# Kernel tuning notes

Measured on AMD Instinct MI355X. Metric: run time of the kernel, lower is better.

The kernel has to match this reference:

```python
import jax, jax.numpy as jnp
import numpy as np

N = 8192      # total nodes = B * NPG
D = 512       # in_dim = hidden_dim = out_dim
E = 131072    # edges
B = 16        # graphs (selected_idx batch)
NPG = 512     # nodes per graph
S = 128       # selected nodes per graph
L = 3         # conv layers
EPS = 1e-5


def setup_inputs() -> dict:
    key = jax.random.key(0)
    ks = jax.random.split(key, 16)
    scale = 0.02
    return {
        "x": jax.random.normal(ks[0], (N, D), dtype=jnp.float32),
        "edge_index": jax.random.randint(ks[1], (2, E), 0, N),
        "selected_idx": jax.random.randint(ks[2], (B, S), 0, NPG),
        "edge_label": jax.random.randint(ks[3], (E,), 0, 4),
        # per-layer EdgeConv MLP params (stacked over L layers)
        "conv_W1": jax.random.normal(ks[4], (L, 2 * D, D), dtype=jnp.float32) * scale,
        "conv_b1": jnp.full((L, D), 0.01, dtype=jnp.float32),
        "conv_W2": jax.random.normal(ks[5], (L, D, D), dtype=jnp.float32) * scale,
        "conv_b2": jnp.full((L, D), 0.01, dtype=jnp.float32),
        # shared layer norms
        "ln1_g": jnp.ones((D,), dtype=jnp.float32),
        "ln1_b": jnp.zeros((D,), dtype=jnp.float32),
        "ln2_g": jnp.ones((D,), dtype=jnp.float32),
        "ln2_b": jnp.zeros((D,), dtype=jnp.float32),
        # final FFN
        "ffn_W1": jax.random.normal(ks[6], (D, D), dtype=jnp.float32) * scale,
        "ffn_b1": jnp.full((D,), 0.01, dtype=jnp.float32),
        "ffn_W2": jax.random.normal(ks[7], (D, D), dtype=jnp.float32) * scale,
        "ffn_b2": jnp.full((D,), 0.01, dtype=jnp.float32),
    }


def _layer_norm(x, g, b):
    mu = jnp.mean(x, axis=-1, keepdims=True)
    var = jnp.mean(jnp.square(x - mu), axis=-1, keepdims=True)
    return (x - mu) * jax.lax.rsqrt(var + EPS) * g + b


def reference(x, edge_index, selected_idx, edge_label,
              conv_W1, conv_b1, conv_W2, conv_b2,
              ln1_g, ln1_b, ln2_g, ln2_b,
              ffn_W1, ffn_b1, ffn_W2, ffn_b2):
    src = edge_index[0]  # x_j source nodes
    dst = edge_index[1]  # x_i target nodes (aggregation index)
    for l in range(L):
        residual = x
        h = _layer_norm(x, ln1_g, ln1_b)
        hi = h[dst]                                   # [E, D]
        hj = h[src]                                   # [E, D]
        ef = jnp.concatenate([hi, hj - hi], axis=1)   # [E, 2D]
        m = jnp.maximum(ef @ conv_W1[l] + conv_b1[l], 0.0) @ conv_W2[l] + conv_b2[l]
        agg = jax.ops.segment_max(m, dst, num_segments=N)  # max-aggregate [N, D]
        agg = jnp.where(jnp.isfinite(agg), agg, 0.0)       # nodes w/o in-edges -> 0
        x = jnp.maximum(agg, 0.0) + residual
    residual = x
    h = _layer_norm(x, ln2_g, ln2_b)
    y = jnp.maximum(h @ ffn_W1 + ffn_b1, 0.0) @ ffn_W2 + ffn_b2
    x = y + residual
    x = x.reshape(B, NPG, D)
    idx = jnp.broadcast_to(selected_idx[:, :, None], (B, S, D))
    return jnp.take_along_axis(x, idx, axis=1)  # [B, S, D]
```

## Files before the change

### kernel.cpp

```cpp
#include <hip/hip_runtime.h>
#include <stdint.h>

#define NN 8192
#define DD 512
#define EE 131072
#define BBATCH 16
#define NPG 512
#define SSEL 128
#define LL 3

typedef unsigned short u16;
typedef __bf16 bf16x8 __attribute__((ext_vector_type(8)));
typedef float f32x4 __attribute__((ext_vector_type(4)));
typedef float f32x2 __attribute__((ext_vector_type(2)));
typedef u16 u16x8 __attribute__((ext_vector_type(8)));

__device__ __forceinline__ float bf2f(u16 u) {
    union { unsigned i; float f; } v; v.i = ((unsigned)u) << 16; return v.f;
}
__device__ __forceinline__ u16 f2bf(float f) {
    union { unsigned i; float f; } v; v.f = f;
    unsigned i = v.i;
    return (u16)((i + 0x7FFFu + ((i >> 16) & 1u)) >> 16);
}

__device__ __forceinline__ unsigned pk_bf16(float s0, float s1) {
#if __has_builtin(__builtin_amdgcn_cvt_pk_bf16_f32)
    typedef __bf16 bf16x2 __attribute__((ext_vector_type(2)));
    union { bf16x2 v; unsigned u; } r;
    r.v = __builtin_amdgcn_cvt_pk_bf16_f32(s0, s1);
    return r.u;
#else
    unsigned r0 = __float_as_uint(s0);
    r0 = (r0 + 0x7FFFu + ((r0 >> 16) & 1u)) >> 16;
    unsigned r1 = __float_as_uint(s1);
    r1 = (r1 + 0x7FFFu + ((r1 >> 16) & 1u)) & 0xffff0000u;
    return r0 | r1;
#endif
}

__device__ __forceinline__ void async_cp16(const u16* g, u16* l) {
    __builtin_amdgcn_global_load_lds(
        (const __attribute__((address_space(1))) unsigned int*)g,
        (__attribute__((address_space(3))) unsigned int*)l, 16, 0, 0);
}

__global__ __launch_bounds__(256) void ln_fused(const float* __restrict__ xin,
                                                float* __restrict__ agg_io,
                                                float* __restrict__ xout,
                                                const float* __restrict__ g,
                                                const float* __restrict__ b,
                                                u16* __restrict__ h, int doAdd) {
    int row = blockIdx.x * 4 + (threadIdx.x >> 6);
    int lane = threadIdx.x & 63;
    const f32x4* x4 = (const f32x4*)(xin + (size_t)row * DD);
    f32x4 p = x4[lane * 2], q = x4[lane * 2 + 1];
    if (doAdd) {
        const f32x4* a4 = (const f32x4*)(agg_io + (size_t)row * DD);
        f32x4 pa = a4[lane * 2], qa = a4[lane * 2 + 1];
        #pragma unroll
        for (int i = 0; i < 4; ++i) { p[i] += pa[i]; q[i] += qa[i]; }
    }
    if (agg_io) {
        f32x4 z;
        #pragma unroll
        for (int i = 0; i < 4; ++i) z[i] = 0.f;
        f32x4* a4 = (f32x4*)(agg_io + (size_t)row * DD);
        a4[lane * 2] = z;
        a4[lane * 2 + 1] = z;
    }
    f32x4* xo = (f32x4*)(xout + (size_t)row * DD);
    xo[lane * 2] = p;
    xo[lane * 2 + 1] = q;
    float v[8];
    v[0] = p[0]; v[1] = p[1]; v[2] = p[2]; v[3] = p[3];
    v[4] = q[0]; v[5] = q[1]; v[6] = q[2]; v[7] = q[3];
    float s = 0.f, sq = 0.f;
    #pragma unroll
    for (int i = 0; i < 8; ++i) { s += v[i]; sq += v[i] * v[i]; }
    #pragma unroll
    for (int o = 32; o >= 1; o >>= 1) { s += __shfl_xor(s, o); sq += __shfl_xor(sq, o); }
    float mu = s * (1.f / DD);
    float var = sq * (1.f / DD) - mu * mu;
    float rs = rsqrtf(var + 1e-5f);
    int kb = lane * 8;
    u16x8 o8;
    #pragma unroll
    for (int i = 0; i < 8; ++i) o8[i] = f2bf((v[i] - mu) * rs * g[kb + i] + b[kb + i]);
    *(u16x8*)(h + (size_t)row * DD + kb) = o8;
}

__global__ __launch_bounds__(256) void ln_sel(const float* __restrict__ x,
                                              const float* __restrict__ agg,
                                              const int* __restrict__ sel,
                                              const float* __restrict__ g,
                                              const float* __restrict__ b,
                                              float* __restrict__ xs,
                                              u16* __restrict__ hs) {
    int i = blockIdx.x * 4 + (threadIdx.x >> 6);
    int lane = threadIdx.x & 63;
    int r = (i >> 7) * NPG + sel[i];
    const f32x4* x4 = (const f32x4*)(x + (size_t)r * DD);
    const f32x4* a4 = (const f32x4*)(agg + (size_t)r * DD);
    f32x4 p = x4[lane * 2], q = x4[lane * 2 + 1];
    f32x4 pa = a4[lane * 2], qa = a4[lane * 2 + 1];
    #pragma unroll
    for (int j = 0; j < 4; ++j) { p[j] += pa[j]; q[j] += qa[j]; }
    f32x4* xo = (f32x4*)(xs + (size_t)i * DD);
    xo[lane * 2] = p;
    xo[lane * 2 + 1] = q;
    float v[8];
    v[0] = p[0]; v[1] = p[1]; v[2] = p[2]; v[3] = p[3];
    v[4] = q[0]; v[5] = q[1]; v[6] = q[2]; v[7] = q[3];
    float s = 0.f, sq = 0.f;
    #pragma unroll
    for (int j = 0; j < 8; ++j) { s += v[j]; sq += v[j] * v[j]; }
    #pragma unroll
    for (int o = 32; o >= 1; o >>= 1) { s += __shfl_xor(s, o); sq += __shfl_xor(sq, o); }
    float mu = s * (1.f / DD);
    float var = sq * (1.f / DD) - mu * mu;
    float rs = rsqrtf(var + 1e-5f);
    int kb = lane * 8;
    u16x8 o8;
    #pragma unroll
    for (int j = 0; j < 8; ++j) o8[j] = f2bf((v[j] - mu) * rs * g[kb + j] + b[kb + j]);
    *(u16x8*)(hs + (size_t)i * DD + kb) = o8;
}

__global__ void hist_kernel(const int* __restrict__ dst, int* __restrict__ cnt) {
    int e = blockIdx.x * 256 + threadIdx.x;
    if (e < EE) atomicAdd(&cnt[dst[e]], 1);
}

__global__ __launch_bounds__(1024) void scan_kernel(const int* __restrict__ cnt,
                                                    int* __restrict__ off,
                                                    int* __restrict__ cur) {
    __shared__ int part[1024];
    int t = threadIdx.x;
    int base = t * 8;
    int loc[8]; int s = 0;
    #pragma unroll
    for (int i = 0; i < 8; ++i) { loc[i] = s; s += cnt[base + i]; }
    part[t] = s;
    __syncthreads();
    for (int o = 1; o < 1024; o <<= 1) {
        int v = part[t];
        int u = (t >= o) ? part[t - o] : 0;
        __syncthreads();
        part[t] = v + u;
        __syncthreads();
    }
    int bx = (t > 0) ? part[t - 1] : 0;
    #pragma unroll
    for (int i = 0; i < 8; ++i) { off[base + i] = bx + loc[i]; cur[base + i] = bx + loc[i]; }
    if (t == 0) off[NN] = part[1023];
}

__global__ void scatter_kernel(const int* __restrict__ src, const int* __restrict__ dst,
                               int* __restrict__ cur, int* __restrict__ ssrc,
                               int* __restrict__ sdst) {
    int e = blockIdx.x * 256 + threadIdx.x;
    if (e < EE) {
        int d = dst[e];
        int p = atomicAdd(&cur[d], 1);
        ssrc[p] = src[e];
        sdst[p] = d;
    }
}

struct CvtJobs {
    const float* s[5];
    u16* d[5];
};
__global__ __launch_bounds__(256) void cvt_t5_kernel(CvtJobs jobs) {
    __shared__ u16 tile[32][33];
    const float* src = jobs.s[blockIdx.z];
    u16* dstp = jobs.d[blockIdx.z];
    int bk = blockIdx.x * 32, bn = blockIdx.y * 32;
    int tx = threadIdx.x & 31, ty = threadIdx.x >> 5;
    #pragma unroll
    for (int r = 0; r < 32; r += 8)
        tile[ty + r][tx] = f2bf(src[(size_t)(bk + ty + r) * 512 + bn + tx]);
    __syncthreads();
    #pragma unroll
    for (int r = 0; r < 32; r += 8)
        dstp[(size_t)(bn + ty + r) * 512 + bk + tx] = tile[tx][ty + r];
}

__global__ __launch_bounds__(256) void cvt_w1_kernel(const float* __restrict__ W1g,
                                                     u16* __restrict__ dstg) {
    __shared__ u16 tile[32][33];
    const float* W1 = W1g + (size_t)blockIdx.z * 1024 * 512;
    u16* dstp = dstg + (size_t)blockIdx.z * 1024 * 512;
    int bk = blockIdx.x * 32, bn = blockIdx.y * 32;
    int tx = threadIdx.x & 31, ty = threadIdx.x >> 5;
    #pragma unroll
    for (int r = 0; r < 32; r += 8) {
        int k = bk + ty + r, n = bn + tx;
        float v = (n < 512) ? (W1[(size_t)k * 512 + n] - W1[(size_t)(k + 512) * 512 + n])
                            : W1[(size_t)(k + 512) * 512 + (n - 512)];
        tile[ty + r][tx] = f2bf(v);
    }
    __syncthreads();
    #pragma unroll
    for (int r = 0; r < 32; r += 8)
        dstp[(size_t)(bn + ty + r) * 512 + bk + tx] = tile[tx][ty + r];
}

template <int EMODE>
__global__ __launch_bounds__(256) void gemm_async(
    const u16* __restrict__ A, const u16* __restrict__ BT,
    const float* __restrict__ bias, const float* __restrict__ resid,
    void* __restrict__ Cout, int K, int ldc) {
    __shared__ u16 lA[128 * 64];
    __shared__ u16 lB[128 * 64];
    const int tid = threadIdx.x;
    const int lane = tid & 63, wave = tid >> 6;
    const int wm = wave & 1, wn = wave >> 1;
    const int quad = lane >> 4, lm = lane & 15;
    const int tileM = blockIdx.x, tileN = blockIdx.y;

    const int g = (lane & 7) ^ (lane >> 3);
    const u16* ap[4];
    const u16* bp[4];
    u16* lad[4];
    u16* lbd[4];
    #pragma unroll
    for (int j = 0; j < 4; ++j) {
        int seg = wave * 4 + j;
        int rA = tileM * 128 + seg * 8 + (lane >> 3);
        int rB = tileN * 128 + seg * 8 + (lane >> 3);
        ap[j] = A + (size_t)rA * K + g * 8;
        bp[j] = BT + (size_t)rB * K + g * 8;
        lad[j] = lA + seg * 512;
        lbd[j] = lB + seg * 512;
    }

    f32x4 acc[4][4];
    #pragma unroll
    for (int mt = 0; mt < 4; ++mt)
        #pragma unroll
        for (int nt = 0; nt < 4; ++nt)
            #pragma unroll
            for (int j = 0; j < 4; ++j) acc[mt][nt][j] = 0.f;

    for (int kb = 0; kb < K; kb += 64) {
        #pragma unroll
        for (int j = 0; j < 4; ++j) {
            async_cp16(ap[j], lad[j]);
            async_cp16(bp[j], lbd[j]);
            ap[j] += 64;
            bp[j] += 64;
        }
        __syncthreads();
        #pragma unroll
        for (int kk = 0; kk < 64; kk += 32) {
            bf16x8 af[4], bfr[4];
            int gbase = (kk >> 3) + quad;
            #pragma unroll
            for (int mt = 0; mt < 4; ++mt) {
                int row = wm * 64 + mt * 16 + lm;
                af[mt] = *(const bf16x8*)(lA + row * 64 + ((gbase ^ (row & 7)) << 3));
            }
            #pragma unroll
            for (int nt = 0; nt < 4; ++nt) {
                int row = wn * 64 + nt * 16 + lm;
                bfr[nt] = *(const bf16x8*)(lB + row * 64 + ((gbase ^ (row & 7)) << 3));
            }
            #pragma unroll
            for (int mt = 0; mt < 4; ++mt)
                #pragma unroll
                for (int nt = 0; nt < 4; ++nt)
                    acc[mt][nt] = __builtin_amdgcn_mfma_f32_16x16x32_bf16(
                        af[mt], bfr[nt], acc[mt][nt], 0, 0, 0);
        }
        __syncthreads();
    }
    #pragma unroll
    for (int mt = 0; mt < 4; ++mt) {
        #pragma unroll
        for (int nt = 0; nt < 4; ++nt) {
            int col = tileN * 128 + wn * 64 + nt * 16 + lm;
            float bv;
            if (EMODE == 2) bv = 0.f;
            else if (EMODE == 3) bv = (col < 512) ? bias[col] : 0.f;
            else bv = bias[col];
            #pragma unroll
            for (int j = 0; j < 4; ++j) {
                int grow = tileM * 128 + wm * 64 + mt * 16 + quad * 4 + j;
                float v = acc[mt][nt][j] + bv;
                if (EMODE == 0) {
                    ((u16*)Cout)[(size_t)grow * ldc + col] = f2bf(fmaxf(v, 0.f));
                } else if (EMODE == 1) {
                    ((float*)Cout)[(size_t)grow * ldc + col] =
                        v + resid[(size_t)grow * ldc + col];
                } else {
                    ((u16*)Cout)[(size_t)grow * ldc + col] = f2bf(v);
                }
            }
        }
    }
}

__global__ __launch_bounds__(1024, 4) void gemm_edge(
    const u16* __restrict__ P, const int* __restrict__ ssrc,
    const int* __restrict__ sdst, const u16* __restrict__ W2T,
    const float* __restrict__ b2, float* __restrict__ agg) {
    __shared__ u16 smem[128 * 64 + 512 * 64];
    __shared__ int nid_l[128];
    u16* lA = smem;
    u16* lB = smem + 128 * 64;
    const int tid = threadIdx.x;
    const int lane = tid & 63, wave = tid >> 6;
    const int wm = wave >> 3, wn = wave & 7;
    const int quad = lane >> 4, lm = lane & 15;
    const int ebase = blockIdx.x * 128;

    if (tid < 128) nid_l[tid] = sdst[ebase + tid];

    const int g = (lane & 7) ^ (lane >> 3);
    int aoff, boff, lout;
    {
        int row = wave * 8 + (lane >> 3);
        int dn = sdst[ebase + row];
        int sn = ssrc[ebase + row];
        aoff = dn * 1024 + g * 8;
        boff = sn * 1024 + 512 + g * 8;
        lout = wave * 512 + lane * 8;
    }
    int wbase, lbbase;
    {
        int row0 = wave * 32 + (lane >> 3);
        wbase = row0 * 512 + g * 8;
        lbbase = wave * 2048;
    }

    f32x4 acc[4][4];
    #pragma unroll
    for (int mt = 0; mt < 4; ++mt)
        #pragma unroll
        for (int nt = 0; nt < 4; ++nt)
            #pragma unroll
            for (int j = 0; j < 4; ++j) acc[mt][nt][j] = 0.f;

    for (int kb = 0; kb < 512; kb += 64) {
        u16x8 ga = *(const u16x8*)(P + aoff + kb);
        u16x8 gb = *(const u16x8*)(P + boff + kb);
        #pragma unroll
        for (int j = 0; j < 4; ++j)
            async_cp16(W2T + wbase + j * 4096 + kb, lB + lbbase + j * 512);
        {
            union { u16x8 v; unsigned w[4]; } ua, ub;
            ua.v = ga;
            ub.v = gb;
            unsigned o[4];
            #pragma unroll
            for (int q = 0; q < 4; ++q) {
                f32x2 a, c;
                a[0] = __uint_as_float(ua.w[q] << 16);
                a[1] = __uint_as_float(ua.w[q] & 0xffff0000u);
                c[0] = __uint_as_float(ub.w[q] << 16);
                c[1] = __uint_as_float(ub.w[q] & 0xffff0000u);
                f32x2 s = a + c;
#if __has_builtin(__builtin_elementwise_max)
                f32x2 z; z[0] = 0.f; z[1] = 0.f;
                s = __builtin_elementwise_max(s, z);
#else
                s[0] = fmaxf(s[0], 0.f);
                s[1] = fmaxf(s[1], 0.f);
#endif
                o[q] = pk_bf16(s[0], s[1]);
            }
            *(uint4*)(lA + lout) = make_uint4(o[0], o[1], o[2], o[3]);
        }
        __syncthreads();
        #pragma unroll
        for (int kk = 0; kk < 64; kk += 32) {
            bf16x8 af[4], bfr[4];
            int gbase = (kk >> 3) + quad;
            #pragma unroll
            for (int mt = 0; mt < 4; ++mt) {
                int row = wm * 64 + mt * 16 + lm;
                af[mt] = *(const bf16x8*)(lA + row * 64 + ((gbase ^ (row & 7)) << 3));
            }
            #pragma unroll
            for (int nt = 0; nt < 4; ++nt) {
                int row = wn * 64 + nt * 16 + lm;
                bfr[nt] = *(const bf16x8*)(lB + row * 64 + ((gbase ^ (row & 7)) << 3));
            }
            #pragma unroll
            for (int mt = 0; mt < 4; ++mt)
                #pragma unroll
                for (int nt = 0; nt < 4; ++nt)
                    acc[mt][nt] = __builtin_amdgcn_mfma_f32_16x16x32_bf16(
                        af[mt], bfr[nt], acc[mt][nt], 0, 0, 0);
        }
        __syncthreads();
    }

    u16* cbuf = smem;
    for (int p = 0; p < 2; ++p) {
        if (wm == p) {
            #pragma unroll
            for (int nt = 0; nt < 4; ++nt) {
                int col = wn * 64 + nt * 16 + lm;
                float bv = b2[col];
                #pragma unroll
                for (int mt = 0; mt < 4; ++mt) {
                    #pragma unroll
                    for (int j2 = 0; j2 < 4; ++j2) {
                        int row = mt * 16 + quad * 4 + j2;
                        cbuf[row * 520 + col] = f2bf(fmaxf(acc[mt][nt][j2] + bv, 0.f));
                    }
                }
            }
        }
        __syncthreads();
        {
            int col = tid & 511;
            int r0 = (tid >> 9) * 32;
            int gr0 = p * 64 + r0;
            int cur = nid_l[gr0];
            float run = bf2f(cbuf[r0 * 520 + col]);
            for (int r = 1; r < 32; ++r) {
                int nd = nid_l[gr0 + r];
                float v = bf2f(cbuf[(r0 + r) * 520 + col]);
                if (nd != cur) {
                    atomicMax((unsigned int*)&agg[(size_t)cur * DD + col],
                              __float_as_uint(run));
                    cur = nd;
                    run = v;
                } else {
                    run = fmaxf(run, v);
                }
            }
            atomicMax((unsigned int*)&agg[(size_t)cur * DD + col],
                      __float_as_uint(run));
        }
        __syncthreads();
    }
}

extern "C" void kernel_launch(void* const* d_in, const int* in_sizes, int n_in,
                              void* d_out, int out_size, void* d_ws, size_t ws_size,
                              hipStream_t stream) {
    const float* x_in = (const float*)d_in[0];
    const int* ei = (const int*)d_in[1];
    const int* sel = (const int*)d_in[2];
    const float* W1 = (const float*)d_in[4];
    const float* b1 = (const float*)d_in[5];
    const float* W2 = (const float*)d_in[6];
    const float* b2 = (const float*)d_in[7];
    const float* g1 = (const float*)d_in[8];
    const float* be1 = (const float*)d_in[9];
    const float* g2 = (const float*)d_in[10];
    const float* be2 = (const float*)d_in[11];
    const float* fW1 = (const float*)d_in[12];
    const float* fb1 = (const float*)d_in[13];
    const float* fW2 = (const float*)d_in[14];
    const float* fb2 = (const float*)d_in[15];
    float* out = (float*)d_out;

    char* w = (char*)d_ws;
    size_t off = 0;
    auto alloc = [&](size_t bytes) -> char* {
        char* p = w + off;
        off += (bytes + 255) & ~(size_t)255;
        return p;
    };
    float* xbuf = (float*)alloc((size_t)NN * DD * 4);
    float* agg  = (float*)alloc((size_t)NN * DD * 4);
    u16* h      = (u16*)alloc((size_t)NN * DD * 2);
    u16* P      = (u16*)alloc((size_t)NN * 1024 * 2);
    u16* W1T    = (u16*)alloc((size_t)LL * 1024 * DD * 2);
    u16* W2T    = (u16*)alloc((size_t)LL * DD * DD * 2);
    u16* FW1T   = (u16*)alloc((size_t)DD * DD * 2);
    u16* FW2T   = (u16*)alloc((size_t)DD * DD * 2);
    int* cnt    = (int*)alloc((size_t)NN * 4);
    int* offs   = (int*)alloc((size_t)(NN + 1) * 4);
    int* cur    = (int*)alloc((size_t)NN * 4);
    int* ssrc   = (int*)alloc((size_t)EE * 4);
    int* sdst   = (int*)alloc((size_t)EE * 4);
    float* xs   = (float*)alloc((size_t)BBATCH * SSEL * DD * 4);
    u16* hs     = (u16*)alloc((size_t)BBATCH * SSEL * DD * 2);
    u16* uu     = (u16*)alloc((size_t)BBATCH * SSEL * DD * 2);

    const int* esrc = ei;
    const int* edst = ei + EE;

    hipMemsetAsync(cnt, 0, (size_t)NN * 4, stream);
    hist_kernel<<<EE / 256, 256, 0, stream>>>(edst, cnt);
    scan_kernel<<<1, 1024, 0, stream>>>(cnt, offs, cur);
    scatter_kernel<<<EE / 256, 256, 0, stream>>>(esrc, edst, cur, ssrc, sdst);

    cvt_w1_kernel<<<dim3(16, 32, LL), 256, 0, stream>>>(W1, W1T);
    {
        CvtJobs jobs;
        jobs.s[0] = W2;
        jobs.s[1] = W2 + (size_t)DD * DD;
        jobs.s[2] = W2 + (size_t)2 * DD * DD;
        jobs.s[3] = fW1;
        jobs.s[4] = fW2;
        jobs.d[0] = W2T;
        jobs.d[1] = W2T + (size_t)DD * DD;
        jobs.d[2] = W2T + (size_t)2 * DD * DD;
        jobs.d[3] = FW1T;
        jobs.d[4] = FW2T;
        cvt_t5_kernel<<<dim3(16, 16, 5), 256, 0, stream>>>(jobs);
    }

    for (int l = 0; l < LL; ++l) {
        ln_fused<<<NN / 4, 256, 0, stream>>>(l == 0 ? x_in : xbuf, agg, xbuf, g1, be1,
                                             h, l > 0 ? 1 : 0);
        {
            dim3 grid(NN / 128, 1024 / 128);
            gemm_async<3><<<grid, 256, 0, stream>>>(
                h, W1T + (size_t)l * 1024 * DD, b1 + (size_t)l * DD, nullptr, P, DD,
                1024);
        }
        gemm_edge<<<EE / 128, 1024, 0, stream>>>(
            P, ssrc, sdst, W2T + (size_t)l * DD * DD, b2 + (size_t)l * DD, agg);
    }

    ln_sel<<<BBATCH * SSEL / 4, 256, 0, stream>>>(xbuf, agg, sel, g2, be2, xs, hs);
    dim3 gridf(BBATCH * SSEL / 128, DD / 128);
    gemm_async<0><<<gridf, 256, 0, stream>>>(hs, FW1T, fb1, nullptr, uu, DD, DD);
    gemm_async<1><<<gridf, 256, 0, stream>>>(uu, FW2T, fb2, xs, out, DD, DD);
}
```

Before: 537.9 us.

## Double-buffer the edge GEMM k-loop with prefetch into alternating LDS buffers

The edge GEMM k-loop now keeps two LDS buffers for the gathered A tile and the W2T tile. The global gathers and async copies for step k+1 are issued before the MFMAs of step k, and the combined A tile is written to the other buffer afterwards. This replaces two __syncthreads per iteration with a single waitcnt plus barrier, so memory latency can overlap with matrix math. The cost is LDS use doubling to the full 160KB per CU, which cuts resident blocks per CU. The node-id scratch array moves into the reused smem region after the loop.

Measured after the change: 668.0 us. 24.2% more time.

```diff
diff --git a/kernel.cpp b/kernel.cpp
--- a/kernel.cpp
+++ b/kernel.cpp
@@ -306,17 +306,14 @@
     const u16* __restrict__ P, const int* __restrict__ ssrc,
     const int* __restrict__ sdst, const u16* __restrict__ W2T,
     const float* __restrict__ b2, float* __restrict__ agg) {
-    __shared__ u16 smem[128 * 64 + 512 * 64];
-    __shared__ int nid_l[128];
+    __shared__ u16 smem[2 * 128 * 64 + 2 * 512 * 64];
     u16* lA = smem;
-    u16* lB = smem + 128 * 64;
+    u16* lB = smem + 2 * 128 * 64;
     const int tid = threadIdx.x;
     const int lane = tid & 63, wave = tid >> 6;
     const int wm = wave >> 3, wn = wave & 7;
     const int quad = lane >> 4, lm = lane & 15;
     const int ebase = blockIdx.x * 128;
-
-    if (tid < 128) nid_l[tid] = sdst[ebase + tid];
 
     const int g = (lane & 7) ^ (lane >> 3);
     int aoff, boff, lout;
@@ -343,37 +340,54 @@
             #pragma unroll
             for (int j = 0; j < 4; ++j) acc[mt][nt][j] = 0.f;
 
-    for (int kb = 0; kb < 512; kb += 64) {
-        u16x8 ga = *(const u16x8*)(P + aoff + kb);
-        u16x8 gb = *(const u16x8*)(P + boff + kb);
-        #pragma unroll
-        for (int j = 0; j < 4; ++j)
-            async_cp16(W2T + wbase + j * 4096 + kb, lB + lbbase + j * 512);
-        {
-            union { u16x8 v; unsigned w[4]; } ua, ub;
-            ua.v = ga;
-            ub.v = gb;
-            unsigned o[4];
-            #pragma unroll
-            for (int q = 0; q < 4; ++q) {
-                f32x2 a, c;
-                a[0] = __uint_as_float(ua.w[q] << 16);
-                a[1] = __uint_as_float(ua.w[q] & 0xffff0000u);
-                c[0] = __uint_as_float(ub.w[q] << 16);
-                c[1] = __uint_as_float(ub.w[q] & 0xffff0000u);
-                f32x2 s = a + c;
+    auto combine_st = [&](u16x8 ga, u16x8 gb, u16* dst) {
+        union { u16x8 v; unsigned w[4]; } ua, ub;
+        ua.v = ga;
+        ub.v = gb;
+        unsigned o[4];
+        #pragma unroll
+        for (int q = 0; q < 4; ++q) {
+            f32x2 a, c;
+            a[0] = __uint_as_float(ua.w[q] << 16);
+            a[1] = __uint_as_float(ua.w[q] & 0xffff0000u);
+            c[0] = __uint_as_float(ub.w[q] << 16);
+            c[1] = __uint_as_float(ub.w[q] & 0xffff0000u);
+            f32x2 s = a + c;
 #if __has_builtin(__builtin_elementwise_max)
-                f32x2 z; z[0] = 0.f; z[1] = 0.f;
-                s = __builtin_elementwise_max(s, z);
+            f32x2 z; z[0] = 0.f; z[1] = 0.f;
+            s = __builtin_elementwise_max(s, z);
 #else
-                s[0] = fmaxf(s[0], 0.f);
-                s[1] = fmaxf(s[1], 0.f);
+            s[0] = fmaxf(s[0], 0.f);
+            s[1] = fmaxf(s[1], 0.f);
 #endif
-                o[q] = pk_bf16(s[0], s[1]);
-            }
-            *(uint4*)(lA + lout) = make_uint4(o[0], o[1], o[2], o[3]);
-        }
-        __syncthreads();
+            o[q] = pk_bf16(s[0], s[1]);
+        }
+        *(uint4*)dst = make_uint4(o[0], o[1], o[2], o[3]);
+    };
+
+    u16x8 ga = *(const u16x8*)(P + aoff);
+    u16x8 gb = *(const u16x8*)(P + boff);
+    #pragma unroll
+    for (int j = 0; j < 4; ++j)
+        async_cp16(W2T + wbase + j * 4096, lB + lbbase + j * 512);
+    combine_st(ga, gb, lA + lout);
+    asm volatile("s_waitcnt vmcnt(0) lgkmcnt(0)" ::: "memory");
+    __builtin_amdgcn_s_barrier();
+
+    #pragma unroll
+    for (int kb = 0; kb < 8; ++kb) {
+        const int cur = kb & 1, nxt = cur ^ 1;
+        const u16* lAc = lA + cur * 8192;
+        const u16* lBc = lB + cur * 32768;
+        if (kb < 7) {
+            ga = *(const u16x8*)(P + aoff + (kb + 1) * 64);
+            gb = *(const u16x8*)(P + boff + (kb + 1) * 64);
+            #pragma unroll
+            for (int j = 0; j < 4; ++j)
+                async_cp16(W2T + wbase + j * 4096 + (kb + 1) * 64,
+                           lB + nxt * 32768 + lbbase + j * 512);
+        }
+        __builtin_amdgcn_sched_barrier(0);
         #pragma unroll
         for (int kk = 0; kk < 64; kk += 32) {
             bf16x8 af[4], bfr[4];
@@ -381,12 +395,12 @@
             #pragma unroll
             for (int mt = 0; mt < 4; ++mt) {
                 int row = wm * 64 + mt * 16 + lm;
-                af[mt] = *(const bf16x8*)(lA + row * 64 + ((gbase ^ (row & 7)) << 3));
+                af[mt] = *(const bf16x8*)(lAc + row * 64 + ((gbase ^ (row & 7)) << 3));
             }
             #pragma unroll
             for (int nt = 0; nt < 4; ++nt) {
                 int row = wn * 64 + nt * 16 + lm;
-                bfr[nt] = *(const bf16x8*)(lB + row * 64 + ((gbase ^ (row & 7)) << 3));
+                bfr[nt] = *(const bf16x8*)(lBc + row * 64 + ((gbase ^ (row & 7)) << 3));
             }
             #pragma unroll
             for (int mt = 0; mt < 4; ++mt)
@@ -395,10 +409,14 @@
                     acc[mt][nt] = __builtin_amdgcn_mfma_f32_16x16x32_bf16(
                         af[mt], bfr[nt], acc[mt][nt], 0, 0, 0);
         }
-        __syncthreads();
+        if (kb < 7) combine_st(ga, gb, lA + nxt * 8192 + lout);
+        asm volatile("s_waitcnt vmcnt(0) lgkmcnt(0)" ::: "memory");
+        __builtin_amdgcn_s_barrier();
     }
 
     u16* cbuf = smem;
+    int* nid_l = (int*)(smem + 128 * 520);
+    if (tid < 128) nid_l[tid] = sdst[ebase + tid];
     for (int p = 0; p < 2; ++p) {
         if (wm == p) {
             #pragma unroll
```
